# Kernel optimization log

Hardware: AMD Instinct MI355X
Metric: run time of the kernel (lower is better)

The kernel has to match this reference:

```python
import jax, jax.numpy as jnp
import numpy as np

EPS = 1e-5

def activation_quant(x):
    # per-token absmax int8 quantization (fake-quant, STE)
    scale = 127.0 / jnp.clip(jnp.max(jnp.abs(x), axis=-1, keepdims=True), EPS, None)
    xq = jnp.clip(jnp.round(x * scale), -128.0, 127.0) / scale
    return x + jax.lax.stop_gradient(xq - x)

def weight_quant(w):
    # per-tensor ternary quantization with mean-abs scale (BitNet b1.58)
    scale = 1.0 / jnp.clip(jnp.mean(jnp.abs(w)), EPS, None)
    wq = jnp.clip(jnp.round(w * scale), -1.0, 1.0) / scale
    return w + jax.lax.stop_gradient(wq - w)

def bitlinear(x, w):
    # w: [out, in]; y = x_q @ w_q^T
    return jnp.einsum('bsd,od->bso', activation_quant(x), weight_quant(w))

def setup_inputs() -> dict:
    key = jax.random.key(0)
    k1, k2, k3 = jax.random.split(key, 3)
    dim, inner = 2048, 8192
    x = jax.random.normal(k1, (4, 2048, dim), dtype=jnp.float32)
    w1 = jax.random.normal(k2, (inner, dim), dtype=jnp.float32) * (dim ** -0.5)
    w2 = jax.random.normal(k3, (dim, inner), dtype=jnp.float32) * (inner ** -0.5)
    return {"x": x, "w1": w1, "w2": w2}

def reference(x, w1, w2):
    h = bitlinear(x, w1)          # [B, S, inner]
    h = jax.nn.relu(h)
    return bitlinear(h, w2)       # [B, S, dim]
```

## Files before the change

### kernel.cpp

```cpp
#include <hip/hip_runtime.h>
#include <hip/hip_bf16.h>
#include <stdint.h>

#define EPSQ 1e-5f

typedef int i32x4 __attribute__((ext_vector_type(4)));

__device__ inline void gload16(const void* g, void* l){
  __builtin_amdgcn_global_load_lds((const __attribute__((address_space(1))) unsigned int*)g,
                                   (__attribute__((address_space(3))) unsigned int*)l, 16, 0, 0);
}

__device__ inline unsigned pack4(float4 v, float s, float lo, float hi){
  int a = (int)fminf(fmaxf(rintf(v.x*s), lo), hi);
  int b = (int)fminf(fmaxf(rintf(v.y*s), lo), hi);
  int c = (int)fminf(fmaxf(rintf(v.z*s), lo), hi);
  int d = (int)fminf(fmaxf(rintf(v.w*s), lo), hi);
  return (unsigned)((a&255)|((b&255)<<8)|((c&255)<<16)|((d&255)<<24));
}

__global__ void absmean2(const float* __restrict__ w1, const float* __restrict__ w2,
                         int n4, double* __restrict__ partial){
  const int half = blockIdx.x >> 10;
  const float4* w4 = (const float4*)(half ? w2 : w1);
  double s = 0.0;
  int idx = (blockIdx.x & 1023)*blockDim.x + threadIdx.x;
  int stride = 1024*blockDim.x;
  for (int i = idx; i < n4; i += stride){
    float4 v = w4[i];
    s += (double)(fabsf(v.x)+fabsf(v.y)+fabsf(v.z)+fabsf(v.w));
  }
  __shared__ double sm[256];
  sm[threadIdx.x] = s; __syncthreads();
  for (int o=128;o>0;o>>=1){ if (threadIdx.x<o) sm[threadIdx.x]+=sm[threadIdx.x+o]; __syncthreads(); }
  if (threadIdx.x==0) partial[blockIdx.x] = sm[0];
}

__global__ void finalize_scales(const double* __restrict__ partial, float* __restrict__ scalebuf, double inv_n){
  __shared__ double sm[256];
  int t = threadIdx.x;
  double s1 = partial[t] + partial[t+256] + partial[t+512] + partial[t+768];
  sm[t]=s1; __syncthreads();
  for(int o=128;o>0;o>>=1){ if(t<o) sm[t]+=sm[t+o]; __syncthreads(); }
  double m1 = sm[0];
  __syncthreads();
  double s2 = partial[1024+t]+partial[1280+t]+partial[1536+t]+partial[1792+t];
  sm[t]=s2; __syncthreads();
  for(int o=128;o>0;o>>=1){ if(t<o) sm[t]+=sm[t+o]; __syncthreads(); }
  if (t==0){
    scalebuf[0] = 1.0f / fmaxf((float)(m1*inv_n),    EPSQ);
    scalebuf[1] = 1.0f / fmaxf((float)(sm[0]*inv_n), EPSQ);
  }
}

__global__ void wquant8(const float* __restrict__ w, char* __restrict__ wq,
                        const float* __restrict__ scalebuf, int which){
  int i = blockIdx.x*256 + threadIdx.x;
  float s = scalebuf[which];
  const float4* w4 = (const float4*)w;
  float4 v0 = w4[(size_t)i*4], v1 = w4[(size_t)i*4+1], v2 = w4[(size_t)i*4+2], v3 = w4[(size_t)i*4+3];
  uint4 pk = make_uint4(pack4(v0,s,-1.f,1.f), pack4(v1,s,-1.f,1.f),
                        pack4(v2,s,-1.f,1.f), pack4(v3,s,-1.f,1.f));
  *reinterpret_cast<uint4*>(wq + (size_t)i*16) = pk;
}

__global__ void aquant8c(const float* __restrict__ x, char* __restrict__ xq,
                         float* __restrict__ s_a, int* __restrict__ rowMax){
  int m = blockIdx.x, t = threadIdx.x;
  if (t==0) rowMax[m] = 0;
  const float4* x4 = (const float4*)(x + (size_t)m*2048);
  float4 a = x4[t*2], b = x4[t*2+1];
  float va[8] = {a.x,a.y,a.z,a.w,b.x,b.y,b.z,b.w};
  float mx = 0.f;
  #pragma unroll
  for (int j=0;j<8;j++) mx = fmaxf(mx, fabsf(va[j]));
  #pragma unroll
  for (int o=1;o<64;o<<=1) mx = fmaxf(mx, __shfl_xor(mx, o, 64));
  __shared__ float wm[4];
  if ((t&63)==0) wm[t>>6] = mx;
  __syncthreads();
  mx = fmaxf(fmaxf(wm[0],wm[1]), fmaxf(wm[2],wm[3]));
  float s = 127.f / fmaxf(mx, EPSQ);
  if (t==0) s_a[m] = s;
  uint2 pk = make_uint2(pack4(a,s,-128.f,127.f), pack4(b,s,-128.f,127.f));
  *reinterpret_cast<uint2*>(xq + (size_t)m*2048 + t*8) = pk;
}

__global__ __launch_bounds__(512,2) void gemm1_256(
    const char* __restrict__ A, const char* __restrict__ B, ushort* __restrict__ C16,
    int* __restrict__ rowMax)
{
  constexpr int STEPS = 16;
  const int Ks = 2048;
  __shared__ __align__(16) char sm[2*65536 + 1024];
  int* smax = (int*)(sm + 2*65536);
  const int tid = threadIdx.x, lane = tid & 63, w = tid >> 6;
  const int wr = w >> 1, wc = w & 1;
  const int n0 = blockIdx.x*256, m0 = blockIdx.y*256;

  i32x4 acc[4][8] = {};

  const int trow = tid >> 3;
  const int scl  = (tid & 7) ^ (trow & 7);
  const char* gA = A + (size_t)(m0 + trow)*Ks + scl*16;
  const char* gB = B + (size_t)(n0 + trow)*Ks + scl*16;

  auto stage = [&](int sbase, int kt){
    #pragma unroll
    for (int i=0;i<4;i++)
      gload16(gA + kt + (size_t)(i*64)*Ks, sm + sbase + (i*512+tid)*16);
    #pragma unroll
    for (int i=0;i<4;i++)
      gload16(gB + kt + (size_t)(i*64)*Ks, sm + sbase + 32768 + (i*512+tid)*16);
  };

  const int frow = lane & 15, kb = lane >> 4;
  int aoff[2][4], boff[2][8];
  #pragma unroll
  for (int kh=0;kh<2;kh++){
    #pragma unroll
    for (int f=0;f<4;f++){
      int ra = wr*64 + f*16 + frow;
      aoff[kh][f] = ra*128 + ((((kh<<2)|kb) ^ (ra&7))<<4);
    }
    #pragma unroll
    for (int f=0;f<8;f++){
      int rb = wc*128 + f*16 + frow;
      boff[kh][f] = 32768 + rb*128 + ((((kh<<2)|kb) ^ (rb&7))<<4);
    }
  }

  auto kstep = [&](const int slot, int t, const int mode){
    const char* base = sm + slot*65536;
    if (mode == 0) stage((slot^1)*65536, (t+1)<<7);
    #pragma unroll
    for (int kh=0;kh<2;kh++){
      i32x4 av[4], bv[8];
      #pragma unroll
      for (int f=0;f<4;f++) av[f] = *reinterpret_cast<const i32x4*>(base + aoff[kh][f]);
      #pragma unroll
      for (int f=0;f<8;f++) bv[f] = *reinterpret_cast<const i32x4*>(base + boff[kh][f]);
      __builtin_amdgcn_s_setprio(1);
      #pragma unroll
      for (int fm=0;fm<4;fm++)
        #pragma unroll
        for (int fn=0;fn<8;fn++)
          acc[fm][fn] = __builtin_amdgcn_mfma_i32_16x16x64_i8(av[fm], bv[fn], acc[fm][fn], 0,0,0);
      __builtin_amdgcn_s_setprio(0);
    }
    if (mode == 0) asm volatile("s_waitcnt vmcnt(0)" ::: "memory");
    if (mode != 2) __builtin_amdgcn_s_barrier();
  };

  stage(0, 0);
  asm volatile("s_waitcnt vmcnt(0)" ::: "memory");
  __builtin_amdgcn_s_barrier();
  __builtin_amdgcn_sched_barrier(0);

  for (int tt = 0; tt < STEPS/2 - 1; ++tt){
    int t = tt*2;
    kstep(0, t,   0);
    kstep(1, t+1, 0);
  }
  kstep(0, STEPS-2, 0);
  kstep(1, STEPS-1, 2);

  const int cc = lane & 15, cr = (lane >> 4)*4;
  __syncthreads();
  if (tid < 256) smax[tid] = 0;
  __syncthreads();
  #pragma unroll
  for (int fm=0;fm<4;fm++){
    #pragma unroll
    for (int reg=0;reg<4;reg++){
      int rl = wr*64 + fm*16 + cr + reg;
      size_t r = (size_t)(m0 + rl);
      int rmax = 0;
      #pragma unroll
      for (int fn=0;fn<8;fn++){
        int v = acc[fm][fn][reg]; v = v > 0 ? v : 0;
        C16[r*8192 + n0 + wc*128 + fn*16 + cc] = (ushort)(v > 65535 ? 65535 : v);
        rmax = v > rmax ? v : rmax;
      }
      atomicMax(&smax[rl], rmax);
    }
  }
  __syncthreads();
  if (tid < 256) atomicMax(&rowMax[m0 + tid], smax[tid]);
}

template<int EPI, int STEPS>
__global__ __launch_bounds__(256,2) void gemmK(
    const char* __restrict__ A, const char* __restrict__ B, void* __restrict__ Cv,
    int moff, int* __restrict__ rowMax, const float* __restrict__ s_a,
    const float* __restrict__ scalebuf)
{
  const int Ks = STEPS << 7;
  __shared__ __align__(16) char sm[2*32768 + 1024];
  int* smax = (int*)(sm + 2*32768);
  const int tid = threadIdx.x, lane = tid & 63, w = tid >> 6;
  const int wr = w >> 1, wc = w & 1;
  const int n0 = blockIdx.x*128, m0 = blockIdx.y*128;

  i32x4 acc[4][4] = {};

  const int trow = tid >> 3;
  const int scl  = (tid & 7) ^ (trow & 7);
  const char* gA = A + (size_t)(m0 + trow)*Ks + scl*16;
  const char* gB = B + (size_t)(n0 + trow)*Ks + scl*16;

  auto stage = [&](int sbase, int kt){
    #pragma unroll
    for (int i=0;i<4;i++){
      gload16(gA + kt + (size_t)(i*32)*Ks, sm + sbase + (i*256+tid)*16);
      gload16(gB + kt + (size_t)(i*32)*Ks, sm + sbase + 16384 + (i*256+tid)*16);
    }
  };

  const int frow = lane & 15, kb = lane >> 4;
  int aoff[2][4], boff[2][4];
  #pragma unroll
  for (int kh=0;kh<2;kh++){
    #pragma unroll
    for (int f=0;f<4;f++){
      int ra = wr*64 + f*16 + frow;
      aoff[kh][f] = ra*128 + ((((kh<<2)|kb) ^ (ra&7))<<4);
      int rb = wc*64 + f*16 + frow;
      boff[kh][f] = 16384 + rb*128 + ((((kh<<2)|kb) ^ (rb&7))<<4);
    }
  }

  auto kstep = [&](const int slot, int t, const int mode){
    const char* base = sm + slot*32768;
    i32x4 av0[4], bv0[4], av1[4], bv1[4];
    #pragma unroll
    for (int f=0;f<4;f++){
      av0[f] = *reinterpret_cast<const i32x4*>(base + aoff[0][f]);
      bv0[f] = *reinterpret_cast<const i32x4*>(base + boff[0][f]);
    }
    #pragma unroll
    for (int f=0;f<4;f++){
      av1[f] = *reinterpret_cast<const i32x4*>(base + aoff[1][f]);
      bv1[f] = *reinterpret_cast<const i32x4*>(base + boff[1][f]);
    }
    if (mode == 0) stage((slot^1)*32768, (t+1)<<7);
    asm volatile("s_waitcnt lgkmcnt(8)" ::: "memory");
    __builtin_amdgcn_sched_barrier(0);
    __builtin_amdgcn_s_setprio(1);
    #pragma unroll
    for (int fm=0;fm<4;fm++)
      #pragma unroll
      for (int fn=0;fn<4;fn++)
        acc[fm][fn] = __builtin_amdgcn_mfma_i32_16x16x64_i8(av0[fm], bv0[fn], acc[fm][fn], 0,0,0);
    __builtin_amdgcn_s_setprio(0);
    asm volatile("s_waitcnt lgkmcnt(0)" ::: "memory");
    __builtin_amdgcn_sched_barrier(0);
    __builtin_amdgcn_s_setprio(1);
    #pragma unroll
    for (int fm=0;fm<4;fm++)
      #pragma unroll
      for (int fn=0;fn<4;fn++)
        acc[fm][fn] = __builtin_amdgcn_mfma_i32_16x16x64_i8(av1[fm], bv1[fn], acc[fm][fn], 0,0,0);
    __builtin_amdgcn_s_setprio(0);
    if (mode == 0) asm volatile("s_waitcnt vmcnt(0)" ::: "memory");
    if (mode != 2) __builtin_amdgcn_s_barrier();
  };

  stage(0, 0);
  asm volatile("s_waitcnt vmcnt(0)" ::: "memory");
  __builtin_amdgcn_s_barrier();
  __builtin_amdgcn_sched_barrier(0);

  for (int tt = 0; tt < STEPS/2 - 1; ++tt){
    int t = tt*2;
    kstep(0, t,   0);
    kstep(1, t+1, 0);
  }
  kstep(0, STEPS-2, 0);
  kstep(1, STEPS-1, 2);

  const int cc = lane & 15, cr = (lane >> 4)*4;
  if (EPI == 0){
    __syncthreads();
    if (tid < 128) smax[tid] = 0;
    __syncthreads();
    ushort* C16 = (ushort*)Cv;
    #pragma unroll
    for (int fm=0;fm<4;fm++){
      #pragma unroll
      for (int reg=0;reg<4;reg++){
        int rl = wr*64 + fm*16 + cr + reg;
        size_t r = (size_t)(m0 + rl);
        int rmax = 0;
        #pragma unroll
        for (int fn=0;fn<4;fn++){
          int v = acc[fm][fn][reg]; v = v > 0 ? v : 0;
          C16[r*8192 + n0 + wc*64 + fn*16 + cc] = (ushort)(v > 65535 ? 65535 : v);
          rmax = v > rmax ? v : rmax;
        }
        atomicMax(&smax[rl], rmax);
      }
    }
    __syncthreads();
    if (tid < 128) atomicMax(&rowMax[m0 + tid], smax[tid]);
  } else {
    float* out = (float*)Cv;
    float sw1 = scalebuf[0], sw2 = scalebuf[1];
    #pragma unroll
    for (int fm=0;fm<4;fm++){
      #pragma unroll
      for (int reg=0;reg<4;reg++){
        int rl = wr*64 + fm*16 + cr + reg;
        size_t r = (size_t)(moff + m0 + rl);
        int Mi = rowMax[r];
        float maxref = (float)Mi / (s_a[r]*sw1);
        float inv2 = fmaxf(maxref, EPSQ) / (127.f*sw2);
        #pragma unroll
        for (int fn=0;fn<4;fn++)
          out[r*2048 + n0 + wc*64 + fn*16 + cc] = (float)acc[fm][fn][reg] * inv2;
      }
    }
  }
}

__global__ void hquant(const ushort* __restrict__ h16, char* __restrict__ hq,
                       const int* __restrict__ rowMax){
  int m = blockIdx.y;
  int Mi = rowMax[m];
  float rqv = (Mi > 0) ? 127.f/(float)Mi : 0.f;
  size_t base = (size_t)m*8192 + blockIdx.x*2048 + threadIdx.x*8;
  uint4 pk = *reinterpret_cast<const uint4*>(h16 + base);
  unsigned u[4] = {pk.x, pk.y, pk.z, pk.w};
  unsigned o[2] = {0,0};
  #pragma unroll
  for (int j=0;j<8;j++){
    float h = (float)(u[j>>1] >> ((j&1)*16) & 0xffff);
    int q = (int)fminf(rintf(h*rqv), 127.f);
    o[j>>2] |= (unsigned)(q & 255) << ((j&3)*8);
  }
  *reinterpret_cast<uint2*>(hq + base) = make_uint2(o[0], o[1]);
}

extern "C" void kernel_launch(void* const* d_in, const int* in_sizes, int n_in,
                              void* d_out, int out_size, void* d_ws, size_t ws_size,
                              hipStream_t stream){
  const float* x  = (const float*)d_in[0];
  const float* w1 = (const float*)d_in[1];
  const float* w2 = (const float*)d_in[2];
  float* out = (float*)d_out;

  const int MTOK = 8192;
  const size_t nW = (size_t)8192*2048;

  char* ws = (char*)d_ws; size_t off = 0;
  auto alloc = [&](size_t n)->char*{ char* p = ws+off; off = (off+n+255) & ~(size_t)255; return p; };

  float*  s_a     = (float*)alloc((size_t)MTOK*4);
  int*    rowMax  = (int*)  alloc((size_t)MTOK*4);
  float*  scalebuf= (float*)alloc(256);
  double* partial = (double*)alloc(2048*8);
  char*   w1q     = alloc(nW);

  bool big = false;
  char *w2q=nullptr, *a8=nullptr, *hq=nullptr;
  ushort* h16=nullptr;
  int hqM = 4096, Mc = 2048;
  if (off + 2*nW  + nW  + 2*nW  + 4096 <= ws_size){
    big = true;
    h16 = (ushort*)alloc(2*nW);
    w2q = (char*)h16;
    a8  = alloc(nW);
    hq  = alloc(2*nW);
  } else {
    Mc = 1024;
    h16 = (ushort*)alloc(nW); w2q = (char*)h16;
    a8  = alloc((size_t)Mc*2048);
    hqM = 0;
    for (int m = 4096; m >= 1024; m >>= 1)
      if (off + (size_t)m*8192 <= ws_size){ hqM = m; break; }
    if (!hqM) return;
    hq = alloc((size_t)hqM*8192);
  }

  absmean2<<<2048,256,0,stream>>>(w1, w2, (int)(nW/4), partial);
  finalize_scales<<<1,256,0,stream>>>(partial, scalebuf, 1.0/(double)nW);
  wquant8<<<(int)(nW/16/256),256,0,stream>>>(w1, w1q, scalebuf, 0);
  if (big) aquant8c<<<MTOK,256,0,stream>>>(x, a8, s_a, rowMax);

  for (int s = 0; s < MTOK/hqM; ++s){
    for (int c = 0; c < hqM/Mc; ++c){
      int ch = s*hqM + c*Mc;
      if (big){
        gemm1_256<<<dim3(32, Mc/256),512,0,stream>>>(
            a8 + (size_t)ch*2048, w1q, h16, rowMax + ch);
      } else {
        aquant8c<<<Mc,256,0,stream>>>(x + (size_t)ch*2048, a8, s_a + ch, rowMax + ch);
        gemmK<0,16><<<dim3(64, Mc/128),256,0,stream>>>(
            a8, w1q, h16, 0, rowMax + ch, nullptr, scalebuf);
      }
      hquant<<<dim3(4, Mc),256,0,stream>>>(h16, hq + (size_t)c*Mc*8192, rowMax + ch);
    }
    wquant8<<<(int)(nW/16/256),256,0,stream>>>(w2, w2q, scalebuf, 1);
    gemmK<1,64><<<dim3(16, hqM/128),256,0,stream>>>(
        hq, w2q, out, s*hqM, rowMax, s_a, scalebuf);
  }
}
```

Before: 363.9 us.

## Replace 256x256 int8 GEMM1 tile with 256x128 tile using fewer waves

Restructures the first int8 GEMM from a 512-thread 256x256 block tile with a 128-wide K step to a 256-thread 256x128 tile with a 64-wide K step. Each of the four waves now covers 64 rows by the full 128 columns, and the LDS swizzle is reworked for 64-byte rows. The grid doubles in N. The aim is lower LDS use and more resident blocks for better latency hiding, at the cost of more reloading of the A tile across blocks and twice as many barriers per K.

```diff
diff --git a/kernel.cpp b/kernel.cpp
--- a/kernel.cpp
+++ b/kernel.cpp
@@ -86,68 +86,59 @@
   *reinterpret_cast<uint2*>(xq + (size_t)m*2048 + t*8) = pk;
 }
 
-__global__ __launch_bounds__(512,2) void gemm1_256(
+__global__ __launch_bounds__(256,2) void gemm1fat(
     const char* __restrict__ A, const char* __restrict__ B, ushort* __restrict__ C16,
     int* __restrict__ rowMax)
 {
-  constexpr int STEPS = 16;
+  constexpr int STEPS = 32;
   const int Ks = 2048;
-  __shared__ __align__(16) char sm[2*65536 + 1024];
-  int* smax = (int*)(sm + 2*65536);
-  const int tid = threadIdx.x, lane = tid & 63, w = tid >> 6;
-  const int wr = w >> 1, wc = w & 1;
-  const int n0 = blockIdx.x*256, m0 = blockIdx.y*256;
+  __shared__ __align__(16) char sm[2*24576 + 1024];
+  int* smax = (int*)(sm + 2*24576);
+  const int tid = threadIdx.x, lane = tid & 63;
+  const int wr = tid >> 6;
+  const int n0 = blockIdx.x*128, m0 = blockIdx.y*256;
 
   i32x4 acc[4][8] = {};
 
-  const int trow = tid >> 3;
-  const int scl  = (tid & 7) ^ (trow & 7);
+  const int trow = tid >> 2;
+  const int scl  = (tid & 3) ^ ((tid >> 3) & 3);
   const char* gA = A + (size_t)(m0 + trow)*Ks + scl*16;
   const char* gB = B + (size_t)(n0 + trow)*Ks + scl*16;
 
   auto stage = [&](int sbase, int kt){
     #pragma unroll
     for (int i=0;i<4;i++)
-      gload16(gA + kt + (size_t)(i*64)*Ks, sm + sbase + (i*512+tid)*16);
-    #pragma unroll
-    for (int i=0;i<4;i++)
-      gload16(gB + kt + (size_t)(i*64)*Ks, sm + sbase + 32768 + (i*512+tid)*16);
+      gload16(gA + kt + (size_t)(i*64)*Ks, sm + sbase + (i*256+tid)*16);
+    #pragma unroll
+    for (int i=0;i<2;i++)
+      gload16(gB + kt + (size_t)(i*64)*Ks, sm + sbase + 16384 + (i*256+tid)*16);
   };
 
   const int frow = lane & 15, kb = lane >> 4;
-  int aoff[2][4], boff[2][8];
-  #pragma unroll
-  for (int kh=0;kh<2;kh++){
-    #pragma unroll
-    for (int f=0;f<4;f++){
-      int ra = wr*64 + f*16 + frow;
-      aoff[kh][f] = ra*128 + ((((kh<<2)|kb) ^ (ra&7))<<4);
-    }
-    #pragma unroll
-    for (int f=0;f<8;f++){
-      int rb = wc*128 + f*16 + frow;
-      boff[kh][f] = 32768 + rb*128 + ((((kh<<2)|kb) ^ (rb&7))<<4);
-    }
-  }
+  const int rkey = ((frow >> 1) & 3);
+  int aoff[4], boff[8];
+  #pragma unroll
+  for (int f=0;f<4;f++)
+    aoff[f] = (wr*64 + f*16 + frow)*64 + ((kb ^ rkey)<<4);
+  #pragma unroll
+  for (int f=0;f<8;f++)
+    boff[f] = 16384 + (f*16 + frow)*64 + ((kb ^ rkey)<<4);
 
   auto kstep = [&](const int slot, int t, const int mode){
-    const char* base = sm + slot*65536;
-    if (mode == 0) stage((slot^1)*65536, (t+1)<<7);
-    #pragma unroll
-    for (int kh=0;kh<2;kh++){
-      i32x4 av[4], bv[8];
-      #pragma unroll
-      for (int f=0;f<4;f++) av[f] = *reinterpret_cast<const i32x4*>(base + aoff[kh][f]);
-      #pragma unroll
-      for (int f=0;f<8;f++) bv[f] = *reinterpret_cast<const i32x4*>(base + boff[kh][f]);
-      __builtin_amdgcn_s_setprio(1);
-      #pragma unroll
-      for (int fm=0;fm<4;fm++)
-        #pragma unroll
-        for (int fn=0;fn<8;fn++)
-          acc[fm][fn] = __builtin_amdgcn_mfma_i32_16x16x64_i8(av[fm], bv[fn], acc[fm][fn], 0,0,0);
-      __builtin_amdgcn_s_setprio(0);
-    }
+    const char* base = sm + slot*24576;
+    if (mode == 0) stage((slot^1)*24576, (t+1)<<6);
+    i32x4 av[4], bv[8];
+    #pragma unroll
+    for (int f=0;f<4;f++) av[f] = *reinterpret_cast<const i32x4*>(base + aoff[f]);
+    #pragma unroll
+    for (int f=0;f<8;f++) bv[f] = *reinterpret_cast<const i32x4*>(base + boff[f]);
+    __builtin_amdgcn_s_setprio(1);
+    #pragma unroll
+    for (int fm=0;fm<4;fm++)
+      #pragma unroll
+      for (int fn=0;fn<8;fn++)
+        acc[fm][fn] = __builtin_amdgcn_mfma_i32_16x16x64_i8(av[fm], bv[fn], acc[fm][fn], 0,0,0);
+    __builtin_amdgcn_s_setprio(0);
     if (mode == 0) asm volatile("s_waitcnt vmcnt(0)" ::: "memory");
     if (mode != 2) __builtin_amdgcn_s_barrier();
   };
@@ -179,7 +170,7 @@
       #pragma unroll
       for (int fn=0;fn<8;fn++){
         int v = acc[fm][fn][reg]; v = v > 0 ? v : 0;
-        C16[r*8192 + n0 + wc*128 + fn*16 + cc] = (ushort)(v > 65535 ? 65535 : v);
+        C16[r*8192 + n0 + fn*16 + cc] = (ushort)(v > 65535 ? 65535 : v);
         rmax = v > rmax ? v : rmax;
       }
       atomicMax(&smax[rl], rmax);
@@ -391,7 +382,7 @@
     for (int c = 0; c < hqM/Mc; ++c){
       int ch = s*hqM + c*Mc;
       if (big){
-        gemm1_256<<<dim3(32, Mc/256),512,0,stream>>>(
+        gemm1fat<<<dim3(64, Mc/256),256,0,stream>>>(
             a8 + (size_t)ch*2048, w1q, h16, rowMax + ch);
       } else {
         aquant8c<<<Mc,256,0,stream>>>(x + (size_t)ch*2048, a8, s_a + ch, rowMax + ch);
```

Result: slower. 380.2 us (+4.5%).
